# Kernel tuning notes

Hardware: AMD Instinct MI355X
Metric: run time of the kernel (lower is better)

## Reference

```python
import jax, jax.numpy as jnp
import numpy as np

N_NODES = 20000
N_EDGES = 160000
EPS = 1e-5
LEAKY_SLOPE = 0.01


def gcn_conv(x, src, dst, W, b, num_nodes):
    """PyG GCNConv: self-loops + symmetric normalization. out = D^-1/2 A_hat D^-1/2 (x W) + b."""
    h = x @ W  # [N, out]
    loop = jnp.arange(num_nodes, dtype=src.dtype)
    s = jnp.concatenate([src, loop])
    d = jnp.concatenate([dst, loop])
    deg = jax.ops.segment_sum(jnp.ones_like(d, dtype=h.dtype), d, num_segments=num_nodes)
    dinv = jnp.where(deg > 0, jax.lax.rsqrt(jnp.maximum(deg, 1.0)) * jnp.where(deg > 0, 1.0, 0.0), 0.0)
    norm = dinv[s] * dinv[d]  # [E+N]
    msgs = h[s] * norm[:, None]  # gather + scale (memory-bound)
    out = jax.ops.segment_sum(msgs, d, num_segments=num_nodes)
    return out + b


def setup_inputs() -> dict:
    key = jax.random.key(0)
    ks = jax.random.split(key, 8)
    x = jax.random.normal(ks[0], (N_NODES, 1), dtype=jnp.float32)
    edge_index = jax.random.randint(ks[1], (2, N_EDGES), 0, N_NODES, dtype=jnp.int32)
    s = 0.02
    W1 = jax.random.normal(ks[2], (1, 2048), dtype=jnp.float32) * s
    b1 = jnp.zeros((2048,), jnp.float32)
    W2 = jax.random.normal(ks[3], (2048, 1024), dtype=jnp.float32) * s
    b2 = jnp.zeros((1024,), jnp.float32)
    gamma = jnp.ones((1024,), jnp.float32)
    beta = jnp.zeros((1024,), jnp.float32)
    running_mean = jnp.zeros((1024,), jnp.float32)
    running_var = jnp.ones((1024,), jnp.float32)
    lW1 = jax.random.normal(ks[4], (1024, 256), dtype=jnp.float32) * s
    lb1 = jnp.zeros((256,), jnp.float32)
    lW2 = jax.random.normal(ks[5], (256, 124), dtype=jnp.float32) * s
    lb2 = jnp.zeros((124,), jnp.float32)
    return dict(x=x, edge_index=edge_index, W1=W1, b1=b1, W2=W2, b2=b2,
                gamma=gamma, beta=beta, running_mean=running_mean,
                running_var=running_var, lW1=lW1, lb1=lb1, lW2=lW2, lb2=lb2)


def reference(x, edge_index, W1, b1, W2, b2, gamma, beta,
              running_mean, running_var, lW1, lb1, lW2, lb2):
    n = x.shape[0]
    src, dst = edge_index[0], edge_index[1]
    h = gcn_conv(x, src, dst, W1, b1, n)          # GCNConv(1, 2048); dropout is identity in eval
    h = gcn_conv(h, src, dst, W2, b2, n)          # GCNConv(2048, 1024)
    h = (h - running_mean) * (gamma * jax.lax.rsqrt(running_var + EPS)) + beta  # BatchNorm (eval)
    h = h @ lW1 + lb1                              # Linear 1024->256
    h = jnp.where(h >= 0, h, LEAKY_SLOPE * h)      # LeakyReLU
    h = h @ lW2 + lb2                              # Linear 256->124
    return jax.nn.log_softmax(h, axis=1)
```

## Files before the change

### kernel.cpp

```cpp
#include <hip/hip_runtime.h>
#include <math.h>

#define N_NODES 20000
#define N_EDGES 160000
#define EPSB 1e-5f
#define SLOPE 0.01f

typedef __attribute__((ext_vector_type(8))) short short8;
typedef __attribute__((ext_vector_type(4))) float f32x4;

#define OFF_DEG    0
#define OFF_V      20000
#define OFF_U      21024
#define OFF_R      22048
#define OFF_RU     22304
#define OFF_S      22560
#define OFF_ZEND   22816
#define OFF_ACC2   22816
#define OFF_B      62816
#define OFF_Q1     82816
#define OFF_BFRAG  122816

#define T_STRIDE 264
#define EQ 40000
#define EQB 157
#define E1_GEMM0 EQB
#define E1_BF0   (EQB + 512)
#define E1_Z0    (EQB + 512 + 16)
#define E1_NB    (EQB + 512 + 16 + 59)

__device__ __forceinline__ unsigned short f2bf(float f) {
    unsigned u = __float_as_uint(f);
    return (unsigned short)((u + 0x7FFFu + ((u >> 16) & 1u)) >> 16);
}

__global__ void E1_deg_v_bf(const int* __restrict__ dst, int* __restrict__ deg,
                            const float* __restrict__ W1, const float* __restrict__ b1,
                            const float* __restrict__ W2, const float* __restrict__ lW2,
                            float* __restrict__ v, float* __restrict__ u,
                            unsigned short* __restrict__ bfrag,
                            float* __restrict__ zbase) {
    int b = blockIdx.x;
    if (b < EQB) {
        int t = b * 256 + threadIdx.x;
        if (t < EQ) {
            int4 d4 = ((const int4*)dst)[t];
            atomicAdd(&deg[d4.x], 1);
            atomicAdd(&deg[d4.y], 1);
            atomicAdd(&deg[d4.z], 1);
            atomicAdd(&deg[d4.w], 1);
        }
    } else if (b < E1_BF0) {
        int bb = b - E1_GEMM0;
        int k  = (bb & 3) * 256 + threadIdx.x;
        int c0 = (bb >> 2) * 16;
        float av = 0.f, au = 0.f;
        for (int c = c0; c < c0 + 16; ++c) {
            float w = W2[c * 1024 + k];
            av = fmaf(W1[c], w, av);
            au = fmaf(b1[c], w, au);
        }
        unsafeAtomicAdd(&v[k], av);
        unsafeAtomicAdd(&u[k], au);
    } else if (b < E1_Z0) {
        int i = (b - E1_BF0) * 256 + threadIdx.x;
        int ct = i >> 9, ks = (i >> 6) & 7, lane = i & 63;
        int n  = ct * 16 + (lane & 15);
        int kb = ks * 32 + (lane >> 4) * 8;
        union { unsigned short u8[8]; short8 v8; } pk;
#pragma unroll
        for (int j = 0; j < 8; ++j)
            pk.u8[j] = (n < 124) ? f2bf(lW2[(kb + j) * 124 + n]) : (unsigned short)0;
        ((short8*)bfrag)[i] = pk.v8;
    } else {
        int i = (b - E1_Z0) * 256 + threadIdx.x;
        if (i < 15000) ((float4*)zbase)[i] = make_float4(0.f, 0.f, 0.f, 0.f);
    }
}

__global__ void E2_edges1_rs_q1(const int* __restrict__ src, const int* __restrict__ dst,
                                const int* __restrict__ deg, const float* __restrict__ x,
                                float* __restrict__ acc2, float2* __restrict__ q1,
                                const float* __restrict__ v, const float* __restrict__ u,
                                const float* __restrict__ gamma, const float* __restrict__ beta,
                                const float* __restrict__ mean, const float* __restrict__ var,
                                const float* __restrict__ b2, const float* __restrict__ lW1,
                                const float* __restrict__ lb1,
                                float* __restrict__ r, float* __restrict__ ru,
                                float* __restrict__ s) {
    int b = blockIdx.x;
    if (b < EQB) {
        int t = b * 256 + threadIdx.x;
        if (t < EQ) {
            int4 s4 = ((const int4*)src)[t];
            int4 d4 = ((const int4*)dst)[t];
            int   g0 = deg[s4.x], g1 = deg[s4.y], g2 = deg[s4.z], g3 = deg[s4.w];
            float x0 = x[s4.x],   x1 = x[s4.y],   x2 = x[s4.z],   x3 = x[s4.w];
            float i0 = rsqrtf((float)(g0 + 1)), i1 = rsqrtf((float)(g1 + 1));
            float i2 = rsqrtf((float)(g2 + 1)), i3 = rsqrtf((float)(g3 + 1));
            unsafeAtomicAdd(&acc2[2 * d4.x],     i0 * x0);
            unsafeAtomicAdd(&acc2[2 * d4.x + 1], i0);
            unsafeAtomicAdd(&acc2[2 * d4.y],     i1 * x1);
            unsafeAtomicAdd(&acc2[2 * d4.y + 1], i1);
            unsafeAtomicAdd(&acc2[2 * d4.z],     i2 * x2);
            unsafeAtomicAdd(&acc2[2 * d4.z + 1], i2);
            unsafeAtomicAdd(&acc2[2 * d4.w],     i3 * x3);
            unsafeAtomicAdd(&acc2[2 * d4.w + 1], i3);
        }
    } else if (b < EQB + 32) {
        int bb = b - EQB, m = threadIdx.x, k0 = bb * 32;
        float ar = 0.f, aru = 0.f, as = 0.f;
        for (int k = k0; k < k0 + 32; ++k) {
            float g = gamma[k] * rsqrtf(var[k] + EPSB);
            float w = lW1[k * 256 + m];
            ar  = fmaf(v[k] * g, w, ar);
            aru = fmaf(u[k] * g, w, aru);
            as  = fmaf(fmaf(b2[k] - mean[k], g, beta[k]), w, as);
        }
        if (bb == 0) as += lb1[m];
        unsafeAtomicAdd(&r[m], ar);
        unsafeAtomicAdd(&ru[m], aru);
        unsafeAtomicAdd(&s[m], as);
    } else {
        int n = (b - (EQB + 32)) * 256 + threadIdx.x;
        if (n < N_NODES) {
            float dinv = rsqrtf((float)(deg[n] + 1));
            float2 q; q.x = dinv * x[n]; q.y = dinv;
            q1[n] = q;
        }
    }
}

__global__ void E3_edges2(const int* __restrict__ src, const int* __restrict__ dst,
                          const float2* __restrict__ q1, const float2* __restrict__ acc2,
                          float* __restrict__ B) {
    int t = blockIdx.x * 256 + threadIdx.x;
    if (t < EQ) {
        int4 s4 = ((const int4*)src)[t];
        int4 d4 = ((const int4*)dst)[t];
        float2 q0 = q1[s4.x], q1v = q1[s4.y], q2v = q1[s4.z], q3 = q1[s4.w];
        float2 a0 = acc2[s4.x], a1 = acc2[s4.y], a2 = acc2[s4.z], a3 = acc2[s4.w];
        unsafeAtomicAdd(&B[d4.x], q0.y  * q0.y  * (a0.x + q0.x));
        unsafeAtomicAdd(&B[d4.y], q1v.y * q1v.y * (a1.x + q1v.x));
        unsafeAtomicAdd(&B[d4.z], q2v.y * q2v.y * (a2.x + q2v.x));
        unsafeAtomicAdd(&B[d4.w], q3.y  * q3.y  * (a3.x + q3.x));
    }
}

__global__ __launch_bounds__(256, 2) void F_final(
    const float2* __restrict__ q1, const float2* __restrict__ acc2,
    const float* __restrict__ B,
    const float* __restrict__ r, const float* __restrict__ ru,
    const float* __restrict__ s,
    const short8* __restrict__ bfrag, const float* __restrict__ lb2,
    float* __restrict__ out) {
    __shared__ unsigned short tsh[16 * T_STRIDE];
    __shared__ float a_sh[16], cn_sh[16];
    __shared__ float logits[16 * 132];
    int tid  = threadIdx.x;
    int lane = tid & 63;
    int wave = __builtin_amdgcn_readfirstlane(tid >> 6);
    int row  = lane & 15, quad = lane >> 4;

    short8 bf0[8], bf1[8];
#pragma unroll
    for (int ks = 0; ks < 8; ++ks) {
        bf0[ks] = bfrag[((wave * 2 + 0) * 8 + ks) * 64 + lane];
        bf1[ks] = bfrag[((wave * 2 + 1) * 8 + ks) * 64 + lane];
    }
    float cr = r[tid], cu = ru[tid], cs = s[tid];

    for (int it = 0; it < 2; ++it) {
        int node0 = (blockIdx.x * 2 + it) * 16;
        if (tid < 16) {
            int n = node0 + tid;
            float2 q  = q1[n];
            float2 ac = acc2[n];
            float dinv = q.y;
            float q2n  = dinv * dinv * (ac.x + q.x);
            a_sh[tid]  = dinv * (B[n] + q2n);
            cn_sh[tid] = dinv * (ac.y + dinv);
        }
        __syncthreads();

#pragma unroll
        for (int n = 0; n < 16; ++n) {
            float t = fmaf(cn_sh[n], cu, fmaf(a_sh[n], cr, cs));
            t = fmaf(SLOPE, fminf(t, 0.f), fmaxf(t, 0.f));
            tsh[n * T_STRIDE + tid] = f2bf(t);
        }
        __syncthreads();

        f32x4 acc0 = {0.f, 0.f, 0.f, 0.f}, acc1 = {0.f, 0.f, 0.f, 0.f};
        const unsigned short* tb = &tsh[row * T_STRIDE + quad * 8];
#pragma unroll
        for (int ks = 0; ks < 8; ++ks) {
            short8 af = *(const short8*)(tb + ks * 32);
            acc0 = __builtin_amdgcn_mfma_f32_16x16x32_bf16(af, bf0[ks], acc0, 0, 0, 0);
            acc1 = __builtin_amdgcn_mfma_f32_16x16x32_bf16(af, bf1[ks], acc1, 0, 0, 0);
        }
        int colbase = wave * 32;
#pragma unroll
        for (int rg = 0; rg < 4; ++rg) {
            int rw = quad * 4 + rg;
            logits[rw * 132 + colbase + row]      = acc0[rg];
            logits[rw * 132 + colbase + 16 + row] = acc1[rg];
        }
        __syncthreads();

        int nd = tid >> 4, sub = tid & 15, c0 = sub * 8;
        int jend = 124 - c0; if (jend > 8) jend = 8;
        float vbuf[8];
        const float* lrow = &logits[nd * 132 + c0];
        float mx = -1e30f;
        for (int j = 0; j < jend; ++j) {
            vbuf[j] = lrow[j] + lb2[c0 + j];
            mx = fmaxf(mx, vbuf[j]);
        }
        mx = fmaxf(mx, __shfl_xor(mx, 1, 16));
        mx = fmaxf(mx, __shfl_xor(mx, 2, 16));
        mx = fmaxf(mx, __shfl_xor(mx, 4, 16));
        mx = fmaxf(mx, __shfl_xor(mx, 8, 16));
        float sm = 0.f;
        for (int j = 0; j < jend; ++j) sm += __expf(vbuf[j] - mx);
        sm += __shfl_xor(sm, 1, 16);
        sm += __shfl_xor(sm, 2, 16);
        sm += __shfl_xor(sm, 4, 16);
        sm += __shfl_xor(sm, 8, 16);
        float lz = mx + __logf(sm);
        float* orow = out + (node0 + nd) * 124 + c0;
        for (int j = 0; j < jend; ++j) orow[j] = vbuf[j] - lz;
    }
}

extern "C" void kernel_launch(void* const* d_in, const int* in_sizes, int n_in,
                              void* d_out, int out_size, void* d_ws, size_t ws_size,
                              hipStream_t stream) {
    const float* x     = (const float*)d_in[0];
    const int*   ei    = (const int*)d_in[1];
    const int*   src   = ei;
    const int*   dst   = ei + N_EDGES;
    const float* W1    = (const float*)d_in[2];
    const float* b1    = (const float*)d_in[3];
    const float* W2    = (const float*)d_in[4];
    const float* b2    = (const float*)d_in[5];
    const float* gamma = (const float*)d_in[6];
    const float* beta  = (const float*)d_in[7];
    const float* rmean = (const float*)d_in[8];
    const float* rvar  = (const float*)d_in[9];
    const float* lW1   = (const float*)d_in[10];
    const float* lb1   = (const float*)d_in[11];
    const float* lW2   = (const float*)d_in[12];
    const float* lb2   = (const float*)d_in[13];
    float* out = (float*)d_out;
    float* ws  = (float*)d_ws;

    int*    deg  = (int*)(ws + OFF_DEG);
    float*  v    = ws + OFF_V;
    float*  u    = ws + OFF_U;
    float*  r    = ws + OFF_R;
    float*  ru   = ws + OFF_RU;
    float*  s    = ws + OFF_S;
    float*  acc2 = ws + OFF_ACC2;
    float*  B    = ws + OFF_B;
    float2* q1   = (float2*)(ws + OFF_Q1);
    unsigned short* bfrag = (unsigned short*)(ws + OFF_BFRAG);

    hipMemsetAsync(ws, 0, OFF_ZEND * sizeof(float), stream);

    E1_deg_v_bf<<<E1_NB, 256, 0, stream>>>(dst, deg, W1, b1, W2, lW2, v, u, bfrag, acc2);
    E2_edges1_rs_q1<<<EQB + 32 + 79, 256, 0, stream>>>(src, dst, deg, x, acc2, q1,
                                                       v, u, gamma, beta, rmean, rvar,
                                                       b2, lW1, lb1, r, ru, s);
    E3_edges2<<<EQB, 256, 0, stream>>>(src, dst, q1, (const float2*)acc2, B);
    F_final<<<625, 256, 0, stream>>>(q1, (const float2*)acc2, B, r, ru, s,
                                     (const short8*)bfrag, lb2, out);
}
```

Baseline: 142.8 us.

## Rebalance independent weight-precompute work across the three edge kernels

The W1·W2 reduction that produces v and u moves from the first kernel to the second, and the lW1 projection that produces r, ru and s moves from the second kernel to the third. This puts each dense precompute alongside a different edge-scatter phase and shrinks the first kernel, so the grid launches are more evenly loaded and the W2 read overlaps with the edge atomics. Dependencies still hold: deg is ready before q1 is computed, and v and u are ready before r and s are computed.

```diff
diff --git a/kernel.cpp b/kernel.cpp
--- a/kernel.cpp
+++ b/kernel.cpp
@@ -24,20 +24,22 @@
 #define T_STRIDE 264
 #define EQ 40000
 #define EQB 157
-#define E1_GEMM0 EQB
-#define E1_BF0   (EQB + 512)
-#define E1_Z0    (EQB + 512 + 16)
-#define E1_NB    (EQB + 512 + 16 + 59)
+
+#define E1_BF0   EQB
+#define E1_Z0    (EQB + 16)
+#define E1_NB    (EQB + 16 + 59)
+#define E2_Q0    EQB
+#define E2_G0    (EQB + 79)
+#define E2_NB    (EQB + 79 + 512)
+#define E3_NB    (EQB + 32)
 
 __device__ __forceinline__ unsigned short f2bf(float f) {
     unsigned u = __float_as_uint(f);
     return (unsigned short)((u + 0x7FFFu + ((u >> 16) & 1u)) >> 16);
 }
 
-__global__ void E1_deg_v_bf(const int* __restrict__ dst, int* __restrict__ deg,
-                            const float* __restrict__ W1, const float* __restrict__ b1,
-                            const float* __restrict__ W2, const float* __restrict__ lW2,
-                            float* __restrict__ v, float* __restrict__ u,
+__global__ void E1_deg_bf_z(const int* __restrict__ dst, int* __restrict__ deg,
+                            const float* __restrict__ lW2,
                             unsigned short* __restrict__ bfrag,
                             float* __restrict__ zbase) {
     int b = blockIdx.x;
@@ -50,18 +52,6 @@
             atomicAdd(&deg[d4.z], 1);
             atomicAdd(&deg[d4.w], 1);
         }
-    } else if (b < E1_BF0) {
-        int bb = b - E1_GEMM0;
-        int k  = (bb & 3) * 256 + threadIdx.x;
-        int c0 = (bb >> 2) * 16;
-        float av = 0.f, au = 0.f;
-        for (int c = c0; c < c0 + 16; ++c) {
-            float w = W2[c * 1024 + k];
-            av = fmaf(W1[c], w, av);
-            au = fmaf(b1[c], w, au);
-        }
-        unsafeAtomicAdd(&v[k], av);
-        unsafeAtomicAdd(&u[k], au);
     } else if (b < E1_Z0) {
         int i = (b - E1_BF0) * 256 + threadIdx.x;
         int ct = i >> 9, ks = (i >> 6) & 7, lane = i & 63;
@@ -78,16 +68,12 @@
     }
 }
 
-__global__ void E2_edges1_rs_q1(const int* __restrict__ src, const int* __restrict__ dst,
+__global__ void E2_edges1_q1_vu(const int* __restrict__ src, const int* __restrict__ dst,
                                 const int* __restrict__ deg, const float* __restrict__ x,
                                 float* __restrict__ acc2, float2* __restrict__ q1,
-                                const float* __restrict__ v, const float* __restrict__ u,
-                                const float* __restrict__ gamma, const float* __restrict__ beta,
-                                const float* __restrict__ mean, const float* __restrict__ var,
-                                const float* __restrict__ b2, const float* __restrict__ lW1,
-                                const float* __restrict__ lb1,
-                                float* __restrict__ r, float* __restrict__ ru,
-                                float* __restrict__ s) {
+                                const float* __restrict__ W1, const float* __restrict__ b1,
+                                const float* __restrict__ W2,
+                                float* __restrict__ v, float* __restrict__ u) {
     int b = blockIdx.x;
     if (b < EQB) {
         int t = b * 256 + threadIdx.x;
@@ -107,7 +93,52 @@
             unsafeAtomicAdd(&acc2[2 * d4.w],     i3 * x3);
             unsafeAtomicAdd(&acc2[2 * d4.w + 1], i3);
         }
-    } else if (b < EQB + 32) {
+    } else if (b < E2_G0) {
+        int n = (b - E2_Q0) * 256 + threadIdx.x;
+        if (n < N_NODES) {
+            float dinv = rsqrtf((float)(deg[n] + 1));
+            float2 q; q.x = dinv * x[n]; q.y = dinv;
+            q1[n] = q;
+        }
+    } else {
+        int bb = b - E2_G0;
+        int k  = (bb & 3) * 256 + threadIdx.x;
+        int c0 = (bb >> 2) * 16;
+        float av = 0.f, au = 0.f;
+        for (int c = c0; c < c0 + 16; ++c) {
+            float w = W2[c * 1024 + k];
+            av = fmaf(W1[c], w, av);
+            au = fmaf(b1[c], w, au);
+        }
+        unsafeAtomicAdd(&v[k], av);
+        unsafeAtomicAdd(&u[k], au);
+    }
+}
+
+__global__ void E3_edges2_rs(const int* __restrict__ src, const int* __restrict__ dst,
+                             const float2* __restrict__ q1, const float2* __restrict__ acc2,
+                             float* __restrict__ B,
+                             const float* __restrict__ v, const float* __restrict__ u,
+                             const float* __restrict__ gamma, const float* __restrict__ beta,
+                             const float* __restrict__ mean, const float* __restrict__ var,
+                             const float* __restrict__ b2, const float* __restrict__ lW1,
+                             const float* __restrict__ lb1,
+                             float* __restrict__ r, float* __restrict__ ru,
+                             float* __restrict__ s) {
+    int b = blockIdx.x;
+    if (b < EQB) {
+        int t = b * 256 + threadIdx.x;
+        if (t < EQ) {
+            int4 s4 = ((const int4*)src)[t];
+            int4 d4 = ((const int4*)dst)[t];
+            float2 q0 = q1[s4.x], q1v = q1[s4.y], q2v = q1[s4.z], q3 = q1[s4.w];
+            float2 a0 = acc2[s4.x], a1 = acc2[s4.y], a2 = acc2[s4.z], a3 = acc2[s4.w];
+            unsafeAtomicAdd(&B[d4.x], q0.y  * q0.y  * (a0.x + q0.x));
+            unsafeAtomicAdd(&B[d4.y], q1v.y * q1v.y * (a1.x + q1v.x));
+            unsafeAtomicAdd(&B[d4.z], q2v.y * q2v.y * (a2.x + q2v.x));
+            unsafeAtomicAdd(&B[d4.w], q3.y  * q3.y  * (a3.x + q3.x));
+        }
+    } else {
         int bb = b - EQB, m = threadIdx.x, k0 = bb * 32;
         float ar = 0.f, aru = 0.f, as = 0.f;
         for (int k = k0; k < k0 + 32; ++k) {
@@ -121,29 +152,6 @@
         unsafeAtomicAdd(&r[m], ar);
         unsafeAtomicAdd(&ru[m], aru);
         unsafeAtomicAdd(&s[m], as);
-    } else {
-        int n = (b - (EQB + 32)) * 256 + threadIdx.x;
-        if (n < N_NODES) {
-            float dinv = rsqrtf((float)(deg[n] + 1));
-            float2 q; q.x = dinv * x[n]; q.y = dinv;
-            q1[n] = q;
-        }
-    }
-}
-
-__global__ void E3_edges2(const int* __restrict__ src, const int* __restrict__ dst,
-                          const float2* __restrict__ q1, const float2* __restrict__ acc2,
-                          float* __restrict__ B) {
-    int t = blockIdx.x * 256 + threadIdx.x;
-    if (t < EQ) {
-        int4 s4 = ((const int4*)src)[t];
-        int4 d4 = ((const int4*)dst)[t];
-        float2 q0 = q1[s4.x], q1v = q1[s4.y], q2v = q1[s4.z], q3 = q1[s4.w];
-        float2 a0 = acc2[s4.x], a1 = acc2[s4.y], a2 = acc2[s4.z], a3 = acc2[s4.w];
-        unsafeAtomicAdd(&B[d4.x], q0.y  * q0.y  * (a0.x + q0.x));
-        unsafeAtomicAdd(&B[d4.y], q1v.y * q1v.y * (a1.x + q1v.x));
-        unsafeAtomicAdd(&B[d4.z], q2v.y * q2v.y * (a2.x + q2v.x));
-        unsafeAtomicAdd(&B[d4.w], q3.y  * q3.y  * (a3.x + q3.x));
     }
 }
 
@@ -268,11 +276,12 @@
 
     hipMemsetAsync(ws, 0, OFF_ZEND * sizeof(float), stream);
 
-    E1_deg_v_bf<<<E1_NB, 256, 0, stream>>>(dst, deg, W1, b1, W2, lW2, v, u, bfrag, acc2);
-    E2_edges1_rs_q1<<<EQB + 32 + 79, 256, 0, stream>>>(src, dst, deg, x, acc2, q1,
-                                                       v, u, gamma, beta, rmean, rvar,
-                                                       b2, lW1, lb1, r, ru, s);
-    E3_edges2<<<EQB, 256, 0, stream>>>(src, dst, q1, (const float2*)acc2, B);
+    E1_deg_bf_z<<<E1_NB, 256, 0, stream>>>(dst, deg, lW2, bfrag, acc2);
+    E2_edges1_q1_vu<<<E2_NB, 256, 0, stream>>>(src, dst, deg, x, acc2, q1,
+                                               W1, b1, W2, v, u);
+    E3_edges2_rs<<<E3_NB, 256, 0, stream>>>(src, dst, q1, (const float2*)acc2, B,
+                                            v, u, gamma, beta, rmean, rvar,
+                                            b2, lW1, lb1, r, ru, s);
     F_final<<<625, 256, 0, stream>>>(q1, (const float2*)acc2, B, r, ru, s,
                                      (const short8*)bfrag, lb2, out);
 }
```

Result: slower. 145.9 us (+2.2%).
